# Kernel optimization log

Hardware: AMD Instinct MI355X
Metric: run time of the kernel (lower is better)

The kernel has to match this reference:

```python
import jax, jax.numpy as jnp
import numpy as np

B, S = 2, 1024
IN, OUT = 1024, 1024
N_IN, N_OUT = 32, 32          # isqrt(IN), isqrt(OUT)
CD = 64                       # compressed_feature_dim
K = 2                         # num_monarchs
D1 = N_IN * N_IN * N_OUT      # 32768, flat M1 size per token
D2 = N_OUT * N_IN * N_OUT     # 32768, flat M2 size per token


def setup_inputs() -> dict:
    key = jax.random.key(0)
    ks = jax.random.split(key, 13)
    g = lambda k, shape, s=0.02: jax.random.normal(k, shape, dtype=jnp.float32) * s
    return {
        "x":  jax.random.normal(ks[0], (B, S, IN), dtype=jnp.float32),
        "Wc": g(ks[1], (IN, CD)),  "bc": g(ks[2], (CD,)),
        "W1": g(ks[3], (K, CD, D1)), "b1": g(ks[4], (K, D1)),
        "W2": g(ks[5], (K, CD, D2)), "b2": g(ks[6], (K, D2)),
        "Wm": g(ks[7], (CD, K)),   "bm": g(ks[8], (K,)),
        "Wb": g(ks[9], (CD, OUT)), "bb": g(ks[10], (OUT,)),
        "Wr": g(ks[11], (CD, 1)),  "br": g(ks[12], (1,)),
    }


def reference(x, Wc, bc, W1, b1, W2, b2, Wm, bm, Wb, bb, Wr, br):
    b, s, _ = x.shape
    # compressor: Linear + Tanh -> [B,S,CD]
    cf = jnp.tanh(x @ Wc + bc)
    # per-expert generated flat weights: [B,S,K,D]
    gen1 = jnp.einsum('bsc,kcd->bskd', cf, W1) + b1
    gen2 = jnp.einsum('bsc,kcd->bskd', cf, W2) + b2
    # expert mixing coefficients -> softmax over K
    coeffs = jax.nn.softmax(cf @ Wm + bm, axis=-1)  # [B,S,K]
    M1f = jnp.einsum('bskd,bsk->bsd', gen1, coeffs)
    M2f = jnp.einsum('bskd,bsk->bsd', gen2, coeffs)
    # Monarch block matmul with per-token weights
    M1 = M1f.reshape(b, s, N_IN, N_IN, N_OUT)   # g=N_IN blocks of [N_IN,N_OUT]
    M2 = M2f.reshape(b, s, N_OUT, N_IN, N_OUT)  # g=N_OUT blocks of [N_IN,N_OUT]
    x1 = x.reshape(b, s, N_IN, N_IN)
    h1 = jnp.einsum('bsgi,bsgio->bsgo', x1, M1)      # [B,S,N_IN,N_OUT]
    h1t = jnp.swapaxes(h1, -1, -2)                   # [B,S,N_OUT,N_IN]
    h2 = jnp.einsum('bsgi,bsgio->bsgo', h1t, M2)     # [B,S,N_OUT,N_OUT]
    y = h2.reshape(b, s, OUT)
    # per-token scale and bias
    ratio = cf @ Wr + br                             # [B,S,1]
    bias = cf @ Wb + bb                              # [B,S,OUT]
    return y * ratio + bias
```

## Files before the change

kernel.cpp:

```cpp
#include <hip/hip_runtime.h>
#include <cstddef>

typedef unsigned short ushortT;
typedef short s8v __attribute__((ext_vector_type(8)));
typedef float f32x4 __attribute__((ext_vector_type(4)));

constexpr int NTOK = 2048;

__device__ inline ushortT f2bf(float f) {
  unsigned u = __float_as_uint(f);
  u += 0x7fffu + ((u >> 16) & 1u);
  return (ushortT)(u >> 16);
}

__device__ inline void gl_lds16(const s8v* g, s8v* l) {
  __builtin_amdgcn_global_load_lds(
      (const __attribute__((address_space(1))) unsigned int*)g,
      (__attribute__((address_space(3))) unsigned int*)l, 16, 0, 0);
}

__global__ __launch_bounds__(256) void setup_kernel(
    const float* __restrict__ x, const float* __restrict__ Wc, const float* __restrict__ bc,
    const float* __restrict__ Wm, const float* __restrict__ bm,
    const float* __restrict__ Wr, const float* __restrict__ br,
    const float* __restrict__ W1, const float* __restrict__ b1,
    const float* __restrict__ W2, const float* __restrict__ b2,
    const float* __restrict__ Wb, const float* __restrict__ bb,
    ushortT* __restrict__ FP, float* __restrict__ ratio,
    ushortT* __restrict__ P1, ushortT* __restrict__ P2, ushortT* __restrict__ WbP)
{
  __shared__ __align__(16) char smem[16384];
  const int tid = threadIdx.x;
  const int bid = blockIdx.x;

  if (bid < 256) {
    float* part = (float*)smem;
    float* cf_s = part + 2048;
    float* a0s  = cf_s + 512;
    float* a1s  = a0s + 8;
    const int c = tid & 63;
    const int q = tid >> 6;
    const int t0 = bid * 8;

    float acc[8];
#pragma unroll
    for (int p = 0; p < 8; ++p) acc[p] = 0.f;
    const float* xq = x + (size_t)t0 * 1024 + q * 256;
    const float* wq = Wc + (size_t)(q * 256) * 64 + c;
#pragma unroll 4
    for (int jj = 0; jj < 64; ++jj) {
      float w0 = wq[(jj * 4 + 0) * 64];
      float w1 = wq[(jj * 4 + 1) * 64];
      float w2 = wq[(jj * 4 + 2) * 64];
      float w3 = wq[(jj * 4 + 3) * 64];
#pragma unroll
      for (int p = 0; p < 8; ++p) {
        float4 xv = *(const float4*)(xq + (size_t)p * 1024 + jj * 4);
        acc[p] = fmaf(xv.x, w0, acc[p]);
        acc[p] = fmaf(xv.y, w1, acc[p]);
        acc[p] = fmaf(xv.z, w2, acc[p]);
        acc[p] = fmaf(xv.w, w3, acc[p]);
      }
    }
#pragma unroll
    for (int p = 0; p < 8; ++p) part[(q * 8 + p) * 64 + c] = acc[p];
    __syncthreads();

#pragma unroll
    for (int r = 0; r < 2; ++r) {
      int idx = tid + r * 256;
      int p = idx >> 6, cc = idx & 63;
      float s = part[(0 * 8 + p) * 64 + cc] + part[(1 * 8 + p) * 64 + cc] +
                part[(2 * 8 + p) * 64 + cc] + part[(3 * 8 + p) * 64 + cc] + bc[cc];
      cf_s[p * 64 + cc] = tanhf(s);
    }
    __syncthreads();

#pragma unroll 1
    for (int pp = 0; pp < 2; ++pp) {
      int p = q * 2 + pp;
      float cf = cf_s[p * 64 + c];
      float z0 = cf * Wm[2 * c], z1 = cf * Wm[2 * c + 1], rr = cf * Wr[c];
      for (int off = 32; off; off >>= 1) {
        z0 += __shfl_down(z0, off);
        z1 += __shfl_down(z1, off);
        rr += __shfl_down(rr, off);
      }
      if (c == 0) {
        z0 += bm[0]; z1 += bm[1];
        float mx = fmaxf(z0, z1);
        float e0 = expf(z0 - mx), e1 = expf(z1 - mx);
        float a0 = e0 / (e0 + e1);
        a0s[p] = a0;
        a1s[p] = 1.0f - a0;
        ratio[t0 + p] = rr + br[0];
      }
    }
    __syncthreads();

    const int ks0 = c >> 5, kk = c & 31;
    const int slot = (kk >> 3) * 16, e = kk & 7;
#pragma unroll
    for (int pp = 0; pp < 2; ++pp) {
      int p = q * 2 + pp;
      int t = t0 + p, tt = t >> 4, tok = t & 15;
      size_t base = (size_t)tt * 2560;
      float cf = cf_s[p * 64 + c];
      float a0 = a0s[p], a1 = a1s[p];
      FP[base + (size_t)ks0 * 512 + (slot + tok) * 8 + e]       = f2bf(a0 * cf);
      FP[base + (size_t)(2 + ks0) * 512 + (slot + tok) * 8 + e] = f2bf(a1 * cf);
      if (c < 32) {
        float v = (c == 0) ? a0 : (c == 1) ? a1 : 0.0f;
        FP[base + 4 * 512 + ((c >> 3) * 16 + tok) * 8 + (c & 7)] = f2bf(v);
      }
    }
  } else {
    ushortT (*lds)[1024] = (ushortT (*)[1024])smem;
    int pb = bid - 256;
    int fac, g, jc8;
    if (pb < 1280) { fac = pb / 640; int rem = pb % 640; g = rem / 20; jc8 = rem % 20; }
    else           { fac = 2; g = 0; jc8 = pb - 1280; }
    const float* W  = (fac == 0) ? W1 : W2;
    const float* bv = (fac == 0) ? b1 : b2;
    ushortT* P = (fac == 0) ? P1 : (fac == 1) ? P2 : WbP;
    const int c4 = tid;

#pragma unroll
    for (int rl = 0; rl < 8; ++rl) {
      int jj = jc8 * 8 + rl;
      float4 v = make_float4(0.f, 0.f, 0.f, 0.f);
      if (fac < 2) {
        if (jj < 128)       v = *(const float4*)(W  + (size_t)jj * 32768 + g * 1024 + c4 * 4);
        else if (jj < 130)  v = *(const float4*)(bv + (size_t)(jj - 128) * 32768 + g * 1024 + c4 * 4);
      } else {
        if (jj < 128)       v = *(const float4*)(Wb + (size_t)(jj & 63) * 1024 + c4 * 4);
        else if (jj < 130)  v = *(const float4*)(bb + c4 * 4);
      }
      int col0 = c4 * 4;
      int sw = col0 ^ ((col0 >> 4) & 0x1C);
      ushortT* d = &lds[rl][sw];
      d[0] = f2bf(v.x); d[1] = f2bf(v.y); d[2] = f2bf(v.z); d[3] = f2bf(v.w);
    }
    __syncthreads();
    const int ks = jc8 >> 2, kkg = jc8 & 3;
#pragma unroll
    for (int it = 0; it < 4; ++it) {
      int idx = tid + it * 256;
      int ct_l = idx >> 4, cl = idx & 15;
      int scol;
      if (fac < 2) {
        int o = ct_l >> 1, ib = (ct_l & 1) * 16;
        scol = (ib + cl) * 32 + o;
      } else {
        scol = ct_l * 16 + cl;
      }
      scol ^= ((scol >> 4) & 0x1C);
      ushortT v[8];
#pragma unroll
      for (int e = 0; e < 8; ++e) v[e] = lds[e][scol];
      size_t ctile = (fac < 2) ? (size_t)(g * 64 + ct_l) : (size_t)ct_l;
      size_t off = ctile * 2560 + (size_t)ks * 512 + (kkg * 16 + cl) * 8;
      uint4 qv;
      qv.x = v[0] | ((unsigned)v[1] << 16);
      qv.y = v[2] | ((unsigned)v[3] << 16);
      qv.z = v[4] | ((unsigned)v[5] << 16);
      qv.w = v[6] | ((unsigned)v[7] << 16);
      *(uint4*)(P + off) = qv;
    }
  }
}

__global__ __launch_bounds__(256) void tr_kernel(
    const float* __restrict__ h1, float* __restrict__ h1x)
{
  __shared__ float lds[8 * 1061];
  const int tid = threadIdx.x, t0 = blockIdx.x * 8;
#pragma unroll
  for (int it = 0; it < 8; ++it) {
    int idx = tid + it * 256;
    int r = idx >> 8, c4 = idx & 255;
    float4 v = *(const float4*)(h1 + (size_t)(t0 + r) * 1024 + c4 * 4);
    int cc = c4 * 4, i = cc >> 5, b0 = cc & 31;
    float* d = lds + r * 1061 + i * 33 + b0;
    d[0] = v.x; d[1] = v.y; d[2] = v.z; d[3] = v.w;
  }
  __syncthreads();
#pragma unroll
  for (int it = 0; it < 8; ++it) {
    int idx = tid + it * 256;
    int g = idx >> 6, rest = idx & 63, r = rest >> 3, i4 = rest & 7;
    float4 v;
    v.x = lds[r * 1061 + (i4 * 4 + 0) * 33 + g];
    v.y = lds[r * 1061 + (i4 * 4 + 1) * 33 + g];
    v.z = lds[r * 1061 + (i4 * 4 + 2) * 33 + g];
    v.w = lds[r * 1061 + (i4 * 4 + 3) * 33 + g];
    *(float4*)(h1x + (size_t)g * 65536 + (size_t)(t0 + r) * 32 + i4 * 4) = v;
  }
}

template <int PASS>
__global__ __launch_bounds__(256, 2) void mm_kernel(
    const s8v* __restrict__ fP, const s8v* __restrict__ wP,
    const s8v* __restrict__ wbP,
    const float* __restrict__ xg,
    const float* __restrict__ rat,
    float* __restrict__ outp)
{
  __shared__ s8v bsh[2][1280];
  __shared__ float xs[64][33];
  __shared__ float hs[64][9];
  __shared__ float bls[PASS == 2 ? 64 : 1][9];
  const int tid = threadIdx.x;
  const int lane = tid & 63;
  const int w = tid >> 6;
  const int bid = blockIdx.x;
  const int cb  = (bid & 7) * 16 + (bid >> 6);
  const int tbg = (bid >> 3) & 7;
  const int g = cb >> 2;

  const s8v* ap = wP + (size_t)(cb * 16 + w * 4) * 320 + lane;
  s8v a[4][5];
#pragma unroll
  for (int i = 0; i < 4; ++i)
#pragma unroll
    for (int ks = 0; ks < 5; ++ks) a[i][ks] = ap[i * 320 + ks * 64];

  s8v ab[5];
  if constexpr (PASS == 2) {
    const s8v* abp = wbP + (size_t)(cb >> 1) * 320 + lane;
#pragma unroll
    for (int ks = 0; ks < 5; ++ks) ab[ks] = abp[ks * 64];
  }

  const s8v* fbase = fP + (size_t)(tbg * 4) * 1280;

#pragma unroll
  for (int c2 = 0; c2 < 5; ++c2)
    gl_lds16(fbase + w * 320 + c2 * 64 + lane, &bsh[0][w * 320 + c2 * 64]);
  __syncthreads();

#pragma unroll 1
  for (int tt2 = 0; tt2 < 4; ++tt2) {
    const int buf = tt2 & 1;
    const int t0 = (tbg * 4 + tt2) * 64;

    float4 xv[2];
#pragma unroll
    for (int it = 0; it < 2; ++it) {
      int idx = tid + it * 256;
      int t = idx >> 3, i4 = idx & 7;
      if (PASS == 1) xv[it] = *(const float4*)(xg + (size_t)(t0 + t) * 1024 + g * 32 + i4 * 4);
      else           xv[it] = *(const float4*)(xg + (size_t)g * 65536 + (size_t)(t0 + t) * 32 + i4 * 4);
    }
    if (tt2 < 3) {
      const s8v* fn = fbase + (size_t)(tt2 + 1) * 1280;
#pragma unroll
      for (int c2 = 0; c2 < 5; ++c2)
        gl_lds16(fn + w * 320 + c2 * 64 + lane, &bsh[buf ^ 1][w * 320 + c2 * 64]);
    }

    f32x4 acc[4][4];
#pragma unroll
    for (int i = 0; i < 4; ++i)
#pragma unroll
      for (int j = 0; j < 4; ++j) acc[i][j] = {0.f, 0.f, 0.f, 0.f};
    f32x4 accb = {0.f, 0.f, 0.f, 0.f};

#pragma unroll
    for (int ks = 0; ks < 5; ++ks) {
      s8v b0 = bsh[buf][0 * 320 + ks * 64 + lane];
      s8v b1 = bsh[buf][1 * 320 + ks * 64 + lane];
      s8v b2 = bsh[buf][2 * 320 + ks * 64 + lane];
      s8v b3 = bsh[buf][3 * 320 + ks * 64 + lane];
      if constexpr (PASS == 2) {
        s8v bw = bsh[buf][w * 320 + ks * 64 + lane];
        accb = __builtin_amdgcn_mfma_f32_16x16x32_bf16(ab[ks], bw, accb, 0, 0, 0);
      }
#pragma unroll
      for (int i = 0; i < 4; ++i) {
        acc[i][0] = __builtin_amdgcn_mfma_f32_16x16x32_bf16(a[i][ks], b0, acc[i][0], 0, 0, 0);
        acc[i][1] = __builtin_amdgcn_mfma_f32_16x16x32_bf16(a[i][ks], b1, acc[i][1], 0, 0, 0);
        acc[i][2] = __builtin_amdgcn_mfma_f32_16x16x32_bf16(a[i][ks], b2, acc[i][2], 0, 0, 0);
        acc[i][3] = __builtin_amdgcn_mfma_f32_16x16x32_bf16(a[i][ks], b3, acc[i][3], 0, 0, 0);
      }
    }

#pragma unroll
    for (int it = 0; it < 2; ++it) {
      int idx = tid + it * 256;
      int t = idx >> 3, i4 = idx & 7;
      float* d = &xs[t][i4 * 4];
      d[0] = xv[it].x; d[1] = xv[it].y; d[2] = xv[it].z; d[3] = xv[it].w;
    }
    __syncthreads();

    const int tau = lane & 15, q = lane >> 4;
#pragma unroll
    for (int tt = 0; tt < 4; ++tt) {
      int tl = tt * 16 + tau;
#pragma unroll
      for (int run = 0; run < 2; ++run) {
        float sacc = 0.f;
#pragma unroll
        for (int ch = 0; ch < 2; ++ch) {
          int ct = run * 2 + ch;
          const float* xp = &xs[tl][ch * 16 + q * 4];
          f32x4 av = acc[ct][tt];
          sacc += av[0] * xp[0] + av[1] * xp[1] + av[2] * xp[2] + av[3] * xp[3];
        }
        sacc += __shfl_xor(sacc, 16);
        sacc += __shfl_xor(sacc, 32);
        if (lane < 16) hs[tl][w * 2 + run] = sacc;
      }
    }
    if constexpr (PASS == 2) {
      if ((lane >> 5) == (cb & 1)) {
        int ol = ((lane >> 4) & 1) * 4;
#pragma unroll
        for (int r = 0; r < 4; ++r) bls[w * 16 + tau][ol + r] = accb[r];
      }
    }
    __syncthreads();

    if (tid < 128) {
      int row = tid >> 1, half = tid & 1;
      int t = t0 + row;
      int col = g * 32 + (cb & 3) * 8 + half * 4;
      float v0 = hs[row][half * 4 + 0], v1 = hs[row][half * 4 + 1];
      float v2 = hs[row][half * 4 + 2], v3 = hs[row][half * 4 + 3];
      float4 o;
      if constexpr (PASS == 2) {
        float r = rat[t];
        o.x = fmaf(v0, r, bls[row][half * 4 + 0]);
        o.y = fmaf(v1, r, bls[row][half * 4 + 1]);
        o.z = fmaf(v2, r, bls[row][half * 4 + 2]);
        o.w = fmaf(v3, r, bls[row][half * 4 + 3]);
      } else {
        o.x = v0; o.y = v1; o.z = v2; o.w = v3;
      }
      *(float4*)(outp + (size_t)t * 1024 + col) = o;
    }
  }
}

extern "C" void kernel_launch(void* const* d_in, const int* in_sizes, int n_in,
                              void* d_out, int out_size, void* d_ws, size_t ws_size,
                              hipStream_t stream) {
  const float* x  = (const float*)d_in[0];
  const float* Wc = (const float*)d_in[1];
  const float* bc = (const float*)d_in[2];
  const float* W1 = (const float*)d_in[3];
  const float* b1 = (const float*)d_in[4];
  const float* W2 = (const float*)d_in[5];
  const float* b2 = (const float*)d_in[6];
  const float* Wm = (const float*)d_in[7];
  const float* bm = (const float*)d_in[8];
  const float* Wb = (const float*)d_in[9];
  const float* bb = (const float*)d_in[10];
  const float* Wr = (const float*)d_in[11];
  const float* br = (const float*)d_in[12];
  float* out = (float*)d_out;

  ushortT* P1  = (ushortT*)d_ws;
  ushortT* P2  = P1 + (size_t)2048 * 2560;
  ushortT* WbP = P2 + (size_t)2048 * 2560;
  ushortT* FP  = WbP + (size_t)64 * 2560;
  float* ratio = (float*)(FP + (size_t)128 * 2560);
  float* h1    = ratio + NTOK;
  float* h1x   = h1 + (size_t)NTOK * 1024;

  setup_kernel<<<dim3(1556), dim3(256), 0, stream>>>(
      x, Wc, bc, Wm, bm, Wr, br, W1, b1, W2, b2, Wb, bb, FP, ratio, P1, P2, WbP);
  mm_kernel<1><<<dim3(1024), dim3(256), 0, stream>>>(
      (const s8v*)FP, (const s8v*)P1, (const s8v*)WbP, x, nullptr, h1);
  tr_kernel<<<dim3(256), dim3(256), 0, stream>>>(h1, h1x);
  mm_kernel<2><<<dim3(1024), dim3(256), 0, stream>>>(
      (const s8v*)FP, (const s8v*)P2, (const s8v*)WbP, h1x, ratio, out);
}
```

Before: 85.78 us.

## Fold h1 transpose into pass-1 store layout and drop transpose kernel

Pass 1 now writes h1 directly in a feature-major [1024][2048] layout, and pass 2 reads it with a matching index scheme and a transposed LDS staging buffer. This removes the separate transpose kernel launch and its full read/write round trip of the 8 MB h1 buffer. In exchange, pass-1 output stores become column-strided float4 writes across tokens, and the LDS access patterns in both passes change, which may add bank conflicts.

```diff
diff --git a/kernel.cpp b/kernel.cpp
--- a/kernel.cpp
+++ b/kernel.cpp
@@ -170,34 +170,6 @@
   }
 }
 
-__global__ __launch_bounds__(256) void tr_kernel(
-    const float* __restrict__ h1, float* __restrict__ h1x)
-{
-  __shared__ float lds[8 * 1061];
-  const int tid = threadIdx.x, t0 = blockIdx.x * 8;
-#pragma unroll
-  for (int it = 0; it < 8; ++it) {
-    int idx = tid + it * 256;
-    int r = idx >> 8, c4 = idx & 255;
-    float4 v = *(const float4*)(h1 + (size_t)(t0 + r) * 1024 + c4 * 4);
-    int cc = c4 * 4, i = cc >> 5, b0 = cc & 31;
-    float* d = lds + r * 1061 + i * 33 + b0;
-    d[0] = v.x; d[1] = v.y; d[2] = v.z; d[3] = v.w;
-  }
-  __syncthreads();
-#pragma unroll
-  for (int it = 0; it < 8; ++it) {
-    int idx = tid + it * 256;
-    int g = idx >> 6, rest = idx & 63, r = rest >> 3, i4 = rest & 7;
-    float4 v;
-    v.x = lds[r * 1061 + (i4 * 4 + 0) * 33 + g];
-    v.y = lds[r * 1061 + (i4 * 4 + 1) * 33 + g];
-    v.z = lds[r * 1061 + (i4 * 4 + 2) * 33 + g];
-    v.w = lds[r * 1061 + (i4 * 4 + 3) * 33 + g];
-    *(float4*)(h1x + (size_t)g * 65536 + (size_t)(t0 + r) * 32 + i4 * 4) = v;
-  }
-}
-
 template <int PASS>
 __global__ __launch_bounds__(256, 2) void mm_kernel(
     const s8v* __restrict__ fP, const s8v* __restrict__ wP,
@@ -207,7 +179,7 @@
     float* __restrict__ outp)
 {
   __shared__ s8v bsh[2][1280];
-  __shared__ float xs[64][33];
+  __shared__ float xsf[2176];
   __shared__ float hs[64][9];
   __shared__ float bls[PASS == 2 ? 64 : 1][9];
   const int tid = threadIdx.x;
@@ -248,9 +220,13 @@
 #pragma unroll
     for (int it = 0; it < 2; ++it) {
       int idx = tid + it * 256;
-      int t = idx >> 3, i4 = idx & 7;
-      if (PASS == 1) xv[it] = *(const float4*)(xg + (size_t)(t0 + t) * 1024 + g * 32 + i4 * 4);
-      else           xv[it] = *(const float4*)(xg + (size_t)g * 65536 + (size_t)(t0 + t) * 32 + i4 * 4);
+      if (PASS == 1) {
+        int t = idx >> 3, i4 = idx & 7;
+        xv[it] = *(const float4*)(xg + (size_t)(t0 + t) * 1024 + g * 32 + i4 * 4);
+      } else {
+        int i = idx >> 4, tq = idx & 15;
+        xv[it] = *(const float4*)(xg + (size_t)(i * 32 + g) * 2048 + t0 + tq * 4);
+      }
     }
     if (tt2 < 3) {
       const s8v* fn = fbase + (size_t)(tt2 + 1) * 1280;
@@ -288,8 +264,9 @@
 #pragma unroll
     for (int it = 0; it < 2; ++it) {
       int idx = tid + it * 256;
-      int t = idx >> 3, i4 = idx & 7;
-      float* d = &xs[t][i4 * 4];
+      float* d;
+      if (PASS == 1) { int t = idx >> 3, i4 = idx & 7; d = &xsf[t * 33 + i4 * 4]; }
+      else           { int i = idx >> 4, tq = idx & 15; d = &xsf[i * 68 + tq * 4]; }
       d[0] = xv[it].x; d[1] = xv[it].y; d[2] = xv[it].z; d[3] = xv[it].w;
     }
     __syncthreads();
@@ -304,9 +281,13 @@
 #pragma unroll
         for (int ch = 0; ch < 2; ++ch) {
           int ct = run * 2 + ch;
-          const float* xp = &xs[tl][ch * 16 + q * 4];
           f32x4 av = acc[ct][tt];
-          sacc += av[0] * xp[0] + av[1] * xp[1] + av[2] * xp[2] + av[3] * xp[3];
+#pragma unroll
+          for (int r = 0; r < 4; ++r) {
+            int i = ch * 16 + q * 4 + r;
+            float xvv = (PASS == 1) ? xsf[tl * 33 + i] : xsf[i * 68 + tl];
+            sacc = fmaf(av[r], xvv, sacc);
+          }
         }
         sacc += __shfl_xor(sacc, 16);
         sacc += __shfl_xor(sacc, 32);
@@ -323,22 +304,27 @@
     __syncthreads();
 
     if (tid < 128) {
-      int row = tid >> 1, half = tid & 1;
-      int t = t0 + row;
-      int col = g * 32 + (cb & 3) * 8 + half * 4;
-      float v0 = hs[row][half * 4 + 0], v1 = hs[row][half * 4 + 1];
-      float v2 = hs[row][half * 4 + 2], v3 = hs[row][half * 4 + 3];
-      float4 o;
-      if constexpr (PASS == 2) {
+      if constexpr (PASS == 1) {
+        int col8 = tid >> 4, tq = tid & 15;
+        int colg = g * 32 + (cb & 3) * 8 + col8;
+        float4 o;
+        o.x = hs[tq * 4 + 0][col8];
+        o.y = hs[tq * 4 + 1][col8];
+        o.z = hs[tq * 4 + 2][col8];
+        o.w = hs[tq * 4 + 3][col8];
+        *(float4*)(outp + (size_t)colg * 2048 + t0 + tq * 4) = o;
+      } else {
+        int row = tid >> 1, half = tid & 1;
+        int t = t0 + row;
+        int col = g * 32 + (cb & 3) * 8 + half * 4;
         float r = rat[t];
-        o.x = fmaf(v0, r, bls[row][half * 4 + 0]);
-        o.y = fmaf(v1, r, bls[row][half * 4 + 1]);
-        o.z = fmaf(v2, r, bls[row][half * 4 + 2]);
-        o.w = fmaf(v3, r, bls[row][half * 4 + 3]);
-      } else {
-        o.x = v0; o.y = v1; o.z = v2; o.w = v3;
-      }
-      *(float4*)(outp + (size_t)t * 1024 + col) = o;
+        float4 o;
+        o.x = fmaf(hs[row][half * 4 + 0], r, bls[row][half * 4 + 0]);
+        o.y = fmaf(hs[row][half * 4 + 1], r, bls[row][half * 4 + 1]);
+        o.z = fmaf(hs[row][half * 4 + 2], r, bls[row][half * 4 + 2]);
+        o.w = fmaf(hs[row][half * 4 + 3], r, bls[row][half * 4 + 3]);
+        *(float4*)(outp + (size_t)t * 1024 + col) = o;
+      }
     }
   }
 }
@@ -366,14 +352,12 @@
   ushortT* WbP = P2 + (size_t)2048 * 2560;
   ushortT* FP  = WbP + (size_t)64 * 2560;
   float* ratio = (float*)(FP + (size_t)128 * 2560);
-  float* h1    = ratio + NTOK;
-  float* h1x   = h1 + (size_t)NTOK * 1024;
+  float* h1T   = ratio + NTOK;
 
   setup_kernel<<<dim3(1556), dim3(256), 0, stream>>>(
       x, Wc, bc, Wm, bm, Wr, br, W1, b1, W2, b2, Wb, bb, FP, ratio, P1, P2, WbP);
   mm_kernel<1><<<dim3(1024), dim3(256), 0, stream>>>(
-      (const s8v*)FP, (const s8v*)P1, (const s8v*)WbP, x, nullptr, h1);
-  tr_kernel<<<dim3(256), dim3(256), 0, stream>>>(h1, h1x);
+      (const s8v*)FP, (const s8v*)P1, (const s8v*)WbP, x, nullptr, h1T);
   mm_kernel<2><<<dim3(1024), dim3(256), 0, stream>>>(
-      (const s8v*)FP, (const s8v*)P2, (const s8v*)WbP, h1x, ratio, out);
-}
+      (const s8v*)FP, (const s8v*)P2, (const s8v*)WbP, h1T, ratio, out);
+}
```

After: 80.46 us. 6.2% less time.
